# Kernel tuning notes

Hardware: AMD Instinct MI355X
Metric: run time of the kernel (lower is better)

Reference implementation:

```python
import jax, jax.numpy as jnp
import numpy as np

H = 128  # GRU hidden size

def gru_cell(x, h, Wih, Whh, bih, bhh):
    # torch GRU gate order: r, z, n
    gx = x @ Wih.T + bih          # (B, 3H)
    gh = h @ Whh.T + bhh          # (B, 3H)
    xr, xz, xn = jnp.split(gx, 3, axis=-1)
    hr, hz, hn = jnp.split(gh, 3, axis=-1)
    r = jax.nn.sigmoid(xr + hr)
    z = jax.nn.sigmoid(xz + hz)
    n = jnp.tanh(xn + r * hn)
    return (1.0 - z) * n + z * h

def conv2d(x, w, b, stride):
    y = jax.lax.conv_general_dilated(x, w, window_strides=(stride, stride), padding='VALID',
                                     dimension_numbers=('NCHW', 'OIHW', 'NCHW'))
    return y + b[None, :, None, None]

def setup_inputs() -> dict:
    key = jax.random.key(0)
    ks = jax.random.split(key, 20)
    B, T = 8192, 64
    s = lambda *sh: 0.1
    inp = {
        'cnn_states': jax.random.normal(ks[0], (B, 8, 8, 27), jnp.float32),
        'linears_states': jax.random.normal(ks[1], (B, T, 29), jnp.float32),
        'conv1_w': jax.random.normal(ks[2], (16, 27, 3, 3), jnp.float32) * 0.1,
        'conv1_b': jnp.zeros((16,), jnp.float32),
        'conv2_w': jax.random.normal(ks[3], (32, 16, 2, 2), jnp.float32) * 0.1,
        'conv2_b': jnp.zeros((32,), jnp.float32),
        'fc_w': jax.random.normal(ks[4], (128, 128), jnp.float32) * 0.1,
        'fc_b': jnp.zeros((128,), jnp.float32),
        'enc_Wih': jax.random.normal(ks[5], (3 * H, 29), jnp.float32) * 0.1,
        'enc_Whh': jax.random.normal(ks[6], (3 * H, H), jnp.float32) * 0.1,
        'enc_bih': jnp.zeros((3 * H,), jnp.float32),
        'enc_bhh': jnp.zeros((3 * H,), jnp.float32),
        'dec_Wih': jax.random.normal(ks[7], (3 * H, H), jnp.float32) * 0.1,
        'dec_Whh': jax.random.normal(ks[8], (3 * H, H), jnp.float32) * 0.1,
        'dec_bih': jnp.zeros((3 * H,), jnp.float32),
        'dec_bhh': jnp.zeros((3 * H,), jnp.float32),
        'dis_w': jax.random.normal(ks[9], (78, 256), jnp.float32) * 0.01,
        'dis_b': jnp.zeros((78,), jnp.float32),
        'value_w': jax.random.normal(ks[10], (1, 256), jnp.float32) * 0.1,
        'value_b': jnp.zeros((1,), jnp.float32),
    }
    return inp

def _forward(cnn_states, linears_states, conv1_w, conv1_b, conv2_w, conv2_b, fc_w, fc_b,
             enc_Wih, enc_Whh, enc_bih, enc_bhh, dec_Wih, dec_Whh, dec_bih, dec_bhh,
             dis_w, dis_b, value_w, value_b):
    B, T = linears_states.shape[0], linears_states.shape[1]
    # CNN encoder (NHWC -> NCHW)
    x = jnp.transpose(cnn_states, (0, 3, 1, 2))
    x = jax.nn.relu(conv2d(x, conv1_w, conv1_b, 2))   # (B,16,3,3)
    x = jax.nn.relu(conv2d(x, conv2_w, conv2_b, 1))   # (B,32,2,2)
    x = x.reshape(B, -1)                               # (B,128), CHW order matches torch Flatten
    z_cnn = jax.nn.relu(x @ fc_w.T + fc_b)             # (B,128)

    # encoder GRU over linears_states
    xs = jnp.transpose(linears_states, (1, 0, 2))      # (T,B,29)
    h0 = jnp.zeros((B, H), linears_states.dtype)
    def enc_step(h, xt):
        h2 = gru_cell(xt, h, enc_Wih, enc_Whh, enc_bih, enc_bhh)
        return h2, None
    h_enc, _ = jax.lax.scan(enc_step, h0, xs)

    x0 = jnp.zeros((B, H), linears_states.dtype)
    def dec_step(carry, _):
        xin, h = carry
        h2 = gru_cell(xin, h, dec_Wih, dec_Whh, dec_bih, dec_bhh)
        return (h2, h2), None
    (z_pn, _), _ = jax.lax.scan(dec_step, (x0, h_enc), None, length=T)

    pn = jnp.concatenate([z_cnn, z_pn], axis=1)        # (B,256)
    distris = pn @ dis_w.T + dis_b                     # (B,78)
    value = pn @ value_w.T + value_b                   # (B,1)
    return distris, value

def reference(cnn_states, linears_states, conv1_w, conv1_b, conv2_w, conv2_b, fc_w, fc_b,
              enc_Wih, enc_Whh, enc_bih, enc_bhh, dec_Wih, dec_Whh, dec_bih, dec_bhh,
              dis_w, dis_b, value_w, value_b):
    return _forward(cnn_states, linears_states, conv1_w, conv1_b, conv2_w, conv2_b, fc_w, fc_b,
                    enc_Wih, enc_Whh, enc_bih, enc_bhh, dec_Wih, dec_Whh, dec_bih, dec_bhh,
                    dis_w, dis_b, value_w, value_b)
```

## Files before the change

kernel.cpp:

```cpp
#include <hip/hip_runtime.h>

typedef _Float16 f16;
typedef _Float16 f16x8 __attribute__((ext_vector_type(8)));
typedef float f32x4 __attribute__((ext_vector_type(4)));

#define WS_EWIH 4194304
#define WS_EWHH 4218880
#define WS_DWC  4317184
#define WS_DWHH 4448256
#define WS_BIAS 4546560
#define WS_W1F  4550656
#define WS_W2F  4559872
#define WS_FCWF 4563968

static __device__ __forceinline__ f32x4 mfma16(f16x8 a, f16x8 b, f32x4 c) {
    return __builtin_amdgcn_mfma_f32_16x16x32_f16(a, b, c, 0, 0, 0);
}
static __device__ __forceinline__ float fexp2n(float x) {
    return __builtin_amdgcn_exp2f(x * -1.4426950408889634f);
}

__global__ void k_prep(const float* __restrict__ eWih, const float* __restrict__ eWhh,
                       const float* __restrict__ ebih, const float* __restrict__ ebhh,
                       const float* __restrict__ dWih, const float* __restrict__ dWhh,
                       const float* __restrict__ dbih, const float* __restrict__ dbhh,
                       const float* __restrict__ w1, const float* __restrict__ w2,
                       const float* __restrict__ fcw,
                       char* __restrict__ ws)
{
    f16* ewih = (f16*)(ws + WS_EWIH);
    f16* ewhh = (f16*)(ws + WS_EWHH);
    f16* dwc  = (f16*)(ws + WS_DWC);
    f16* dwhh = (f16*)(ws + WS_DWHH);
    float* bias = (float*)(ws + WS_BIAS);
    f16* w1f = (f16*)(ws + WS_W1F);
    f16* w2f = (f16*)(ws + WS_W2F);
    f16* fcwf = (f16*)(ws + WS_FCWF);
    const int total = 12288 + 49152 + 65536 + 49152 + 1024 + 4608 + 2048 + 16384;
    for (int i = blockIdx.x * 256 + threadIdx.x; i < total; i += gridDim.x * 256) {
        int j = i;
        if (j < 12288) { int g = j >> 5, k = j & 31;
            ewih[j] = (f16)((k < 29) ? eWih[g * 29 + k] : 0.0f); continue; }
        j -= 12288;
        if (j < 49152) { ewhh[j] = (f16)eWhh[j]; continue; }
        j -= 49152;
        if (j < 65536) { int row = j >> 7, k = j & 127; float v;
            if (row < 256)      v = dWih[row * 128 + k] + dWhh[row * 128 + k];
            else if (row < 384) v = dWih[row * 128 + k];
            else                v = dWhh[(row - 128) * 128 + k];
            dwc[j] = (f16)v; continue; }
        j -= 65536;
        if (j < 49152) { dwhh[j] = (f16)dWhh[j]; continue; }
        j -= 49152;
        if (j < 1024) {
            if (j < 256)        bias[j] = ebih[j] + ebhh[j];
            else if (j < 384)   bias[j] = ebih[j];
            else if (j < 512)   bias[j] = ebhh[j - 128];
            else if (j < 768)   bias[j] = dbih[j - 512] + dbhh[j - 512];
            else if (j < 896)   bias[j] = dbih[j - 512];
            else                bias[j] = dbhh[j - 640];
            continue; }
        j -= 1024;
        if (j < 4608) {
            int kk = j >> 9, rem = j & 511, co = rem >> 5, k = rem & 31;
            w1f[j] = (f16)((k < 27) ? w1[co * 243 + k * 9 + kk] : 0.0f); continue; }
        j -= 4608;
        if (j < 2048) {
            int s = j >> 10, rem = j & 1023, co = rem >> 5, k = rem & 31;
            int kk2 = 2 * s + (k >= 16), ci = k & 15;
            w2f[j] = (f16)w2[co * 64 + ci * 4 + kk2]; continue; }
        j -= 2048;
        fcwf[j] = (f16)fcw[j];
    }
}

__global__ __launch_bounds__(512, 4) void k_gru(
    const float* __restrict__ cin,
    const float* __restrict__ lin,
    const float* __restrict__ b1, const float* __restrict__ b2,
    const float* __restrict__ fcb,
    const char* __restrict__ ws,
    const float* __restrict__ dis_w, const float* __restrict__ dis_b,
    const float* __restrict__ value_w, const float* __restrict__ value_b,
    float* __restrict__ out)
{
    __shared__ __align__(16) char smem[31488];
    f16 (*a1f)[9][24]  = (f16(*)[9][24])(smem);
    f16 (*x_s)[16][32] = (f16(*)[16][32])(smem + 8192);
    float (*pn_s)[264] = (float(*)[264])(smem + 10240);
    f16 (*vf)[136]     = (f16(*)[136])(smem + 27136);
#define HS(B) (smem + (B) * 4096)

    const int tid = threadIdx.x;
    const int wv = tid >> 6;
    const int lane = tid & 63;
    const int nl = lane & 15;
    const int quad = lane >> 4;
    const int j0 = wv * 16;
    const int row0 = blockIdx.x * 16;

    const f16* ewih = (const f16*)(ws + WS_EWIH);
    const f16* ewhh = (const f16*)(ws + WS_EWHH);
    const f16* dwc  = (const f16*)(ws + WS_DWC);
    const f16* dwhh = (const f16*)(ws + WS_DWHH);
    const float* bias = (const float*)(ws + WS_BIAS);
    const f16* w1f = (const f16*)(ws + WS_W1F);
    const f16* w2f = (const f16*)(ws + WS_W2F);
    const f16* fcwf = (const f16*)(ws + WS_FCWF);

    {
        const float* imgp = cin + (size_t)(row0 + nl) * 1728 + quad * 8;
        float b1v = b1[nl];
        for (int p = wv; p < 9; p += 8) {
            int oy = p / 3, ox = p % 3;
            f32x4 acc = {b1v, b1v, b1v, b1v};
            #pragma unroll
            for (int kk = 0; kk < 9; kk++) {
                f16x8 bw = *(const f16x8*)(w1f + (kk * 16 + nl) * 32 + quad * 8);
                int pix = (2 * oy + kk / 3) * 8 + (2 * ox + kk % 3);
                const float* s = imgp + pix * 27;
                f16x8 a;
                #pragma unroll
                for (int jj = 0; jj < 8; jj++) a[jj] = (f16)s[jj];
                acc = mfma16(a, bw, acc);
            }
            #pragma unroll
            for (int r = 0; r < 4; r++)
                a1f[quad * 4 + r][p][nl] = (f16)fmaxf(acc[r], 0.0f);
        }
        __syncthreads();
        {
            int pos = wv >> 1, nt = wv & 1;
            int y = pos >> 1, x = pos & 1;
            float bv = b2[nt * 16 + nl];
            f32x4 acc = {bv, bv, bv, bv};
            #pragma unroll
            for (int s = 0; s < 2; s++) {
                int kk2 = 2 * s + (quad >> 1);
                int pos1 = (y + (kk2 >> 1)) * 3 + (x + (kk2 & 1));
                f16x8 a = *(const f16x8*)(&a1f[nl][pos1][(quad & 1) * 8]);
                f16x8 b = *(const f16x8*)(w2f + ((size_t)s * 32 + nt * 16 + nl) * 32 + quad * 8);
                acc = mfma16(a, b, acc);
            }
            #pragma unroll
            for (int r = 0; r < 4; r++)
                vf[quad * 4 + r][(nt * 16 + nl) * 4 + (y * 2 + x)] = (f16)fmaxf(acc[r], 0.0f);
        }
        __syncthreads();
        {
            int o = wv * 16 + nl;
            float bv = fcb[o];
            f32x4 acc = {bv, bv, bv, bv};
            #pragma unroll
            for (int kt = 0; kt < 4; kt++) {
                f16x8 a = *(const f16x8*)(&vf[nl][kt * 32 + quad * 8]);
                f16x8 b = *(const f16x8*)(fcwf + o * 128 + kt * 32 + quad * 8);
                acc = mfma16(a, b, acc);
            }
            #pragma unroll
            for (int r = 0; r < 4; r++)
                pn_s[quad * 4 + r][o] = fmaxf(acc[r], 0.0f);
        }
        __syncthreads();
    }

    for (int i = tid; i < 4096; i += 512) ((f16*)smem)[i] = (f16)0.0f;

    const int lane7 = nl & 7;
    int rb[4], wb[4];
    #pragma unroll
    for (int kt = 0; kt < 4; kt++)
        rb[kt] = nl * 256 + (((4 * kt + quad) ^ lane7) << 4);
    #pragma unroll
    for (int r = 0; r < 4; r++) {
        int row = quad * 4 + r;
        wb[r] = row * 256 + ((((2 * wv + (nl >> 3)) ^ (row & 7)) << 3) + lane7) * 2;
    }

    float ho[4];
    #pragma unroll
    for (int r = 0; r < 4; r++) ho[r] = 0.0f;

    const int xr = tid >> 5, xc = tid & 31;
    const bool xok = (xc < 29);
    const size_t lin_base = (size_t)(row0 + xr) * 1856 + xc;

    {
        float eb_r, eb_z, eb_xn, eb_hn;
        { int c = j0 + nl;
          eb_r = bias[c]; eb_z = bias[128 + c]; eb_xn = bias[256 + c]; eb_hn = bias[384 + c]; }
        f16x8 we_r[4], we_z[4], we_hn[4], we_xr, we_xz, we_xn;
        { int gr = j0 + nl;
          #pragma unroll
          for (int kt = 0; kt < 4; kt++) {
              we_r[kt]  = *(const f16x8*)(ewhh + gr * 128 + kt * 32 + quad * 8);
              we_z[kt]  = *(const f16x8*)(ewhh + (128 + gr) * 128 + kt * 32 + quad * 8);
              we_hn[kt] = *(const f16x8*)(ewhh + (256 + gr) * 128 + kt * 32 + quad * 8);
          }
          we_xr = *(const f16x8*)(ewih + gr * 32 + quad * 8);
          we_xz = *(const f16x8*)(ewih + (128 + gr) * 32 + quad * 8);
          we_xn = *(const f16x8*)(ewih + (256 + gr) * 32 + quad * 8);
        }

        float xv = xok ? lin[lin_base] : 0.0f;

#define ENC_STEP(BUF, OBUF, TN)                                                      \
        do {                                                                         \
            x_s[BUF][xr][xc] = (f16)xv;                                              \
            __syncthreads();                                                         \
            f16x8 ax = *(const f16x8*)(&x_s[BUF][nl][quad * 8]);                     \
            f16x8 ah0 = *(const f16x8*)(HS(BUF) + rb[0]);                            \
            f16x8 ah1 = *(const f16x8*)(HS(BUF) + rb[1]);                            \
            f16x8 ah2 = *(const f16x8*)(HS(BUF) + rb[2]);                            \
            f16x8 ah3 = *(const f16x8*)(HS(BUF) + rb[3]);                            \
            if ((TN) < 64) xv = xok ? lin[lin_base + (TN) * 29] : 0.0f;              \
            f32x4 aR  = {eb_r, eb_r, eb_r, eb_r};                                    \
            f32x4 aZ  = {eb_z, eb_z, eb_z, eb_z};                                    \
            f32x4 aXN = {eb_xn, eb_xn, eb_xn, eb_xn};                                \
            f32x4 aHN = {eb_hn, eb_hn, eb_hn, eb_hn};                                \
            aR  = mfma16(ax, we_xr, aR);                                             \
            aZ  = mfma16(ax, we_xz, aZ);                                             \
            aXN = mfma16(ax, we_xn, aXN);                                            \
            aR  = mfma16(ah0, we_r[0], aR);  aR  = mfma16(ah1, we_r[1], aR);         \
            aR  = mfma16(ah2, we_r[2], aR);  aR  = mfma16(ah3, we_r[3], aR);         \
            aZ  = mfma16(ah0, we_z[0], aZ);  aZ  = mfma16(ah1, we_z[1], aZ);         \
            aZ  = mfma16(ah2, we_z[2], aZ);  aZ  = mfma16(ah3, we_z[3], aZ);         \
            aHN = mfma16(ah0, we_hn[0], aHN); aHN = mfma16(ah1, we_hn[1], aHN);      \
            aHN = mfma16(ah2, we_hn[2], aHN); aHN = mfma16(ah3, we_hn[3], aHN);      \
            _Pragma("unroll")                                                        \
            for (int r = 0; r < 4; r++) {                                            \
                float ea = fexp2n(aR[r]), eb = fexp2n(aZ[r]);                        \
                float s1 = 1.0f + ea, s2 = 1.0f + eb;                                \
                float R = __builtin_amdgcn_rcpf(s1 * s2);                            \
                float rg = s2 * R, zg = s1 * R;                                      \
                float ec = fexp2n(2.0f * (aXN[r] + rg * aHN[r]));                    \
                float ng = (1.0f - ec) * __builtin_amdgcn_rcpf(1.0f + ec);           \
                float h = ng + zg * (ho[r] - ng);                                    \
                ho[r] = h;                                                           \
                *(f16*)(HS(OBUF) + wb[r]) = (f16)h;                                  \
            }                                                                        \
        } while (0)

        for (int t = 0; t < 64; t += 2) {
            ENC_STEP(0, 1, t + 1);
            ENC_STEP(1, 0, t + 2);
        }
#undef ENC_STEP
    }

    float db_r, db_z, db_xn, db_hn;
    { int c = j0 + nl;
      db_r = bias[512 + c]; db_z = bias[640 + c]; db_xn = bias[768 + c]; db_hn = bias[896 + c]; }

    {
        __syncthreads();
        f16x8 ah0 = *(const f16x8*)(HS(0) + rb[0]);
        f16x8 ah1 = *(const f16x8*)(HS(0) + rb[1]);
        f16x8 ah2 = *(const f16x8*)(HS(0) + rb[2]);
        f16x8 ah3 = *(const f16x8*)(HS(0) + rb[3]);
        int gr = j0 + nl;
        f32x4 aR  = {db_r, db_r, db_r, db_r};
        f32x4 aZ  = {db_z, db_z, db_z, db_z};
        f32x4 aHN = {db_hn, db_hn, db_hn, db_hn};
        #pragma unroll
        for (int kt = 0; kt < 4; kt++) {
            f16x8 b0 = *(const f16x8*)(dwhh + gr * 128 + kt * 32 + quad * 8);
            f16x8 b1 = *(const f16x8*)(dwhh + (128 + gr) * 128 + kt * 32 + quad * 8);
            f16x8 b2 = *(const f16x8*)(dwhh + (256 + gr) * 128 + kt * 32 + quad * 8);
            f16x8 a = (kt == 0) ? ah0 : (kt == 1) ? ah1 : (kt == 2) ? ah2 : ah3;
            aR  = mfma16(a, b0, aR);
            aZ  = mfma16(a, b1, aZ);
            aHN = mfma16(a, b2, aHN);
        }
        #pragma unroll
        for (int r = 0; r < 4; r++) {
            float ea = fexp2n(aR[r]), eb = fexp2n(aZ[r]);
            float s1 = 1.0f + ea, s2 = 1.0f + eb;
            float R = __builtin_amdgcn_rcpf(s1 * s2);
            float rg = s2 * R, zg = s1 * R;
            float ec = fexp2n(2.0f * (db_xn + rg * aHN[r]));
            float ng = (1.0f - ec) * __builtin_amdgcn_rcpf(1.0f + ec);
            float h = ng + zg * (ho[r] - ng);
            ho[r] = h;
            *(f16*)(HS(1) + wb[r]) = (f16)h;
        }
    }
    {
        f16x8 wd_r[4], wd_z[4], wd_xn[4], wd_hn[4];
        { int gr = j0 + nl;
          #pragma unroll
          for (int kt = 0; kt < 4; kt++) {
              wd_r[kt]  = *(const f16x8*)(dwc + gr * 128 + kt * 32 + quad * 8);
              wd_z[kt]  = *(const f16x8*)(dwc + (128 + gr) * 128 + kt * 32 + quad * 8);
              wd_xn[kt] = *(const f16x8*)(dwc + (256 + gr) * 128 + kt * 32 + quad * 8);
              wd_hn[kt] = *(const f16x8*)(dwc + (384 + gr) * 128 + kt * 32 + quad * 8);
          }
        }

#define DEC_STEP(BUF, OBUF)                                                          \
        do {                                                                         \
            __syncthreads();                                                         \
            f16x8 ah0 = *(const f16x8*)(HS(BUF) + rb[0]);                            \
            f16x8 ah1 = *(const f16x8*)(HS(BUF) + rb[1]);                            \
            f16x8 ah2 = *(const f16x8*)(HS(BUF) + rb[2]);                            \
            f16x8 ah3 = *(const f16x8*)(HS(BUF) + rb[3]);                            \
            f32x4 aR  = {db_r, db_r, db_r, db_r};                                    \
            f32x4 aZ  = {db_z, db_z, db_z, db_z};                                    \
            f32x4 aXN = {db_xn, db_xn, db_xn, db_xn};                                \
            f32x4 aHN = {db_hn, db_hn, db_hn, db_hn};                                \
            aR  = mfma16(ah0, wd_r[0], aR);   aR  = mfma16(ah1, wd_r[1], aR);        \
            aR  = mfma16(ah2, wd_r[2], aR);   aR  = mfma16(ah3, wd_r[3], aR);        \
            aZ  = mfma16(ah0, wd_z[0], aZ);   aZ  = mfma16(ah1, wd_z[1], aZ);        \
            aZ  = mfma16(ah2, wd_z[2], aZ);   aZ  = mfma16(ah3, wd_z[3], aZ);        \
            aXN = mfma16(ah0, wd_xn[0], aXN); aXN = mfma16(ah1, wd_xn[1], aXN);      \
            aXN = mfma16(ah2, wd_xn[2], aXN); aXN = mfma16(ah3, wd_xn[3], aXN);      \
            aHN = mfma16(ah0, wd_hn[0], aHN); aHN = mfma16(ah1, wd_hn[1], aHN);      \
            aHN = mfma16(ah2, wd_hn[2], aHN); aHN = mfma16(ah3, wd_hn[3], aHN);      \
            _Pragma("unroll")                                                        \
            for (int r = 0; r < 4; r++) {                                            \
                float ea = fexp2n(aR[r]), eb = fexp2n(aZ[r]);                        \
                float s1 = 1.0f + ea, s2 = 1.0f + eb;                                \
                float R = __builtin_amdgcn_rcpf(s1 * s2);                            \
                float rg = s2 * R, zg = s1 * R;                                      \
                float ec = fexp2n(2.0f * (aXN[r] + rg * aHN[r]));                    \
                float ng = (1.0f - ec) * __builtin_amdgcn_rcpf(1.0f + ec);           \
                float h = ng + zg * (ho[r] - ng);                                    \
                ho[r] = h;                                                           \
                *(f16*)(HS(OBUF) + wb[r]) = (f16)h;                                  \
            }                                                                        \
        } while (0)

        DEC_STEP(1, 0);
        for (int t = 2; t < 64; t += 2) {
            DEC_STEP(0, 1);
            DEC_STEP(1, 0);
        }
#undef DEC_STEP
    }

    #pragma unroll
    for (int r = 0; r < 4; r++)
        pn_s[quad * 4 + r][128 + j0 + nl] = ho[r];
    __syncthreads();

    const int rr = tid & 15, og = tid >> 4;
    const float4* pr4 = (const float4*)(&pn_s[rr][0]);
    for (int o = og; o < 79; o += 32) {
        const float* wrow_p = (o < 78) ? (dis_w + o * 256) : value_w;
        float acc = (o < 78) ? dis_b[o] : value_b[0];
        const float4* wr4 = (const float4*)wrow_p;
        #pragma unroll 8
        for (int k = 0; k < 64; k++) {
            float4 a = wr4[k], b = pr4[k];
            acc += a.x * b.x + a.y * b.y + a.z * b.z + a.w * b.w;
        }
        if (o < 78) out[(size_t)(row0 + rr) * 78 + o] = acc;
        else        out[(size_t)8192 * 78 + row0 + rr] = acc;
    }
#undef HS
}

extern "C" void kernel_launch(void* const* d_in, const int* in_sizes, int n_in,
                              void* d_out, int out_size, void* d_ws, size_t ws_size,
                              hipStream_t stream)
{
    (void)in_sizes; (void)n_in; (void)out_size; (void)ws_size;
    const float* cnn  = (const float*)d_in[0];
    const float* lin  = (const float*)d_in[1];
    const float* c1w  = (const float*)d_in[2];
    const float* c1b  = (const float*)d_in[3];
    const float* c2w  = (const float*)d_in[4];
    const float* c2b  = (const float*)d_in[5];
    const float* fcw  = (const float*)d_in[6];
    const float* fcb  = (const float*)d_in[7];
    const float* eWih = (const float*)d_in[8];
    const float* eWhh = (const float*)d_in[9];
    const float* ebih = (const float*)d_in[10];
    const float* ebhh = (const float*)d_in[11];
    const float* dWih = (const float*)d_in[12];
    const float* dWhh = (const float*)d_in[13];
    const float* dbih = (const float*)d_in[14];
    const float* dbhh = (const float*)d_in[15];
    const float* disw = (const float*)d_in[16];
    const float* disb = (const float*)d_in[17];
    const float* vw   = (const float*)d_in[18];
    const float* vb   = (const float*)d_in[19];
    char* ws = (char*)d_ws;
    float* out = (float*)d_out;

    hipLaunchKernelGGL(k_prep, dim3(128), dim3(256), 0, stream,
                       eWih, eWhh, ebih, ebhh, dWih, dWhh, dbih, dbhh,
                       c1w, c2w, fcw, ws);
    hipLaunchKernelGGL(k_gru, dim3(512), dim3(512), 0, stream,
                       cnn, lin, c1b, c2b, fcb, ws, disw, disb, vw, vb, out);
}
```

Before: 334.4 us.

## Stage GRU weight fragments through shared memory with coalesced loads

```diff
diff --git a/kernel.cpp b/kernel.cpp
--- a/kernel.cpp
+++ b/kernel.cpp
@@ -74,7 +74,7 @@
     }
 }
 
-__global__ __launch_bounds__(512, 4) void k_gru(
+__global__ __launch_bounds__(512, 2) void k_gru(
     const float* __restrict__ cin,
     const float* __restrict__ lin,
     const float* __restrict__ b1, const float* __restrict__ b2,
@@ -84,11 +84,12 @@
     const float* __restrict__ value_w, const float* __restrict__ value_b,
     float* __restrict__ out)
 {
-    __shared__ __align__(16) char smem[31488];
+    __shared__ __align__(16) char smem[47360];
     f16 (*a1f)[9][24]  = (f16(*)[9][24])(smem);
     f16 (*x_s)[16][32] = (f16(*)[16][32])(smem + 8192);
+    char* wstage       = smem + 10240;
     float (*pn_s)[264] = (float(*)[264])(smem + 10240);
-    f16 (*vf)[136]     = (f16(*)[136])(smem + 27136);
+    f16 (*vf)[136]     = (f16(*)[136])(smem + 43008);
 #define HS(B) (smem + (B) * 4096)
 
     const int tid = threadIdx.x;
@@ -107,6 +108,8 @@
     const f16* w1f = (const f16*)(ws + WS_W1F);
     const f16* w2f = (const f16*)(ws + WS_W2F);
     const f16* fcwf = (const f16*)(ws + WS_FCWF);
+
+    float zc[4];
 
     {
         const float* imgp = cin + (size_t)(row0 + nl) * 1728 + quad * 8;
@@ -159,7 +162,7 @@
             }
             #pragma unroll
             for (int r = 0; r < 4; r++)
-                pn_s[quad * 4 + r][o] = fmaxf(acc[r], 0.0f);
+                zc[r] = fmaxf(acc[r], 0.0f);
         }
         __syncthreads();
     }
@@ -177,6 +180,8 @@
         wb[r] = row * 256 + ((((2 * wv + (nl >> 3)) ^ (row & 7)) << 3) + lane7) * 2;
     }
 
+    const int frag_off0 = ((j0 + nl) * 128) * 2 + (quad * 8) * 2;
+
     float ho[4];
     #pragma unroll
     for (int r = 0; r < 4; r++) ho[r] = 0.0f;
@@ -189,17 +194,32 @@
         float eb_r, eb_z, eb_xn, eb_hn;
         { int c = j0 + nl;
           eb_r = bias[c]; eb_z = bias[128 + c]; eb_xn = bias[256 + c]; eb_hn = bias[384 + c]; }
+
         f16x8 we_r[4], we_z[4], we_hn[4], we_xr, we_xz, we_xn;
-        { int gr = j0 + nl;
-          #pragma unroll
-          for (int kt = 0; kt < 4; kt++) {
-              we_r[kt]  = *(const f16x8*)(ewhh + gr * 128 + kt * 32 + quad * 8);
-              we_z[kt]  = *(const f16x8*)(ewhh + (128 + gr) * 128 + kt * 32 + quad * 8);
-              we_hn[kt] = *(const f16x8*)(ewhh + (256 + gr) * 128 + kt * 32 + quad * 8);
-          }
-          we_xr = *(const f16x8*)(ewih + gr * 32 + quad * 8);
-          we_xz = *(const f16x8*)(ewih + (128 + gr) * 32 + quad * 8);
-          we_xn = *(const f16x8*)(ewih + (256 + gr) * 32 + quad * 8);
+        {
+            __syncthreads();
+            for (int i = tid * 16; i < 24576; i += 512 * 16)
+                *(f16x8*)(wstage + i) = *(const f16x8*)((const char*)ewih + i);
+            __syncthreads();
+            we_xr = *(const f16x8*)(wstage + ((j0 + nl) * 32 + quad * 8) * 2);
+            we_xz = *(const f16x8*)(wstage + ((128 + j0 + nl) * 32 + quad * 8) * 2);
+            we_xn = *(const f16x8*)(wstage + ((256 + j0 + nl) * 32 + quad * 8) * 2);
+            #pragma unroll
+            for (int g = 0; g < 3; g++) {
+                __syncthreads();
+                const char* src = (const char*)(ewhh + g * 128 * 128);
+                for (int i = tid * 16; i < 32768; i += 512 * 16)
+                    *(f16x8*)(wstage + i) = *(const f16x8*)(src + i);
+                __syncthreads();
+                #pragma unroll
+                for (int kt = 0; kt < 4; kt++) {
+                    f16x8 v = *(const f16x8*)(wstage + frag_off0 + kt * 64);
+                    if (g == 0) we_r[kt] = v;
+                    else if (g == 1) we_z[kt] = v;
+                    else we_hn[kt] = v;
+                }
+            }
+            __syncthreads();
         }
 
         float xv = xok ? lin[lin_base] : 0.0f;
@@ -287,14 +307,21 @@
     }
     {
         f16x8 wd_r[4], wd_z[4], wd_xn[4], wd_hn[4];
-        { int gr = j0 + nl;
-          #pragma unroll
-          for (int kt = 0; kt < 4; kt++) {
-              wd_r[kt]  = *(const f16x8*)(dwc + gr * 128 + kt * 32 + quad * 8);
-              wd_z[kt]  = *(const f16x8*)(dwc + (128 + gr) * 128 + kt * 32 + quad * 8);
-              wd_xn[kt] = *(const f16x8*)(dwc + (256 + gr) * 128 + kt * 32 + quad * 8);
-              wd_hn[kt] = *(const f16x8*)(dwc + (384 + gr) * 128 + kt * 32 + quad * 8);
-          }
+        #pragma unroll
+        for (int g = 0; g < 4; g++) {
+            __syncthreads();
+            const char* src = (const char*)(dwc + g * 128 * 128);
+            for (int i = tid * 16; i < 32768; i += 512 * 16)
+                *(f16x8*)(wstage + i) = *(const f16x8*)(src + i);
+            __syncthreads();
+            #pragma unroll
+            for (int kt = 0; kt < 4; kt++) {
+                f16x8 v = *(const f16x8*)(wstage + frag_off0 + kt * 64);
+                if (g == 0) wd_r[kt] = v;
+                else if (g == 1) wd_z[kt] = v;
+                else if (g == 2) wd_xn[kt] = v;
+                else wd_hn[kt] = v;
+            }
         }
 
 #define DEC_STEP(BUF, OBUF)                                                          \
@@ -338,9 +365,12 @@
 #undef DEC_STEP
     }
 
+    __syncthreads();
     #pragma unroll
-    for (int r = 0; r < 4; r++)
+    for (int r = 0; r < 4; r++) {
+        pn_s[quad * 4 + r][wv * 16 + nl] = zc[r];
         pn_s[quad * 4 + r][128 + j0 + nl] = ho[r];
+    }
     __syncthreads();
 
     const int rr = tid & 15, og = tid >> 4;
```

Measured after the change: 369.3 us. +10.4%, slower.

## Process two independent 16-row batch tiles per block to interleave GRU recurrences

Applied to the files above, without the earlier changes.

```diff
diff --git a/kernel.cpp b/kernel.cpp
--- a/kernel.cpp
+++ b/kernel.cpp
@@ -74,7 +74,7 @@
     }
 }
 
-__global__ __launch_bounds__(512, 4) void k_gru(
+__global__ __launch_bounds__(512, 2) void k_gru(
     const float* __restrict__ cin,
     const float* __restrict__ lin,
     const float* __restrict__ b1, const float* __restrict__ b2,
@@ -84,12 +84,14 @@
     const float* __restrict__ value_w, const float* __restrict__ value_b,
     float* __restrict__ out)
 {
-    __shared__ __align__(16) char smem[31488];
+    __shared__ __align__(16) char smem[62976];
     f16 (*a1f)[9][24]  = (f16(*)[9][24])(smem);
-    f16 (*x_s)[16][32] = (f16(*)[16][32])(smem + 8192);
-    float (*pn_s)[264] = (float(*)[264])(smem + 10240);
-    f16 (*vf)[136]     = (f16(*)[136])(smem + 27136);
-#define HS(B) (smem + (B) * 4096)
+    float (*pn_s)[264] = (float(*)[264])(smem + 20480);
+    f16 (*vf)[136]     = (f16(*)[136])(smem + 54272);
+#define HSA(B) (smem + (B) * 4096)
+#define HSB(B) (smem + 8192 + (B) * 4096)
+#define XSA(B) ((f16(*)[32])(smem + 16384 + (B) * 1024))
+#define XSB(B) ((f16(*)[32])(smem + 18432 + (B) * 1024))
 
     const int tid = threadIdx.x;
     const int wv = tid >> 6;
@@ -97,7 +99,7 @@
     const int nl = lane & 15;
     const int quad = lane >> 4;
     const int j0 = wv * 16;
-    const int row0 = blockIdx.x * 16;
+    const int row0 = blockIdx.x * 32;
 
     const f16* ewih = (const f16*)(ws + WS_EWIH);
     const f16* ewhh = (const f16*)(ws + WS_EWHH);
@@ -108,11 +110,14 @@
     const f16* w2f = (const f16*)(ws + WS_W2F);
     const f16* fcwf = (const f16*)(ws + WS_FCWF);
 
+    float zc[2][4];
+
     {
-        const float* imgp = cin + (size_t)(row0 + nl) * 1728 + quad * 8;
         float b1v = b1[nl];
-        for (int p = wv; p < 9; p += 8) {
+        for (int p2 = wv; p2 < 18; p2 += 8) {
+            int g = p2 / 9, p = p2 % 9;
             int oy = p / 3, ox = p % 3;
+            const float* imgp = cin + (size_t)(row0 + g * 16 + nl) * 1728 + quad * 8;
             f32x4 acc = {b1v, b1v, b1v, b1v};
             #pragma unroll
             for (int kk = 0; kk < 9; kk++) {
@@ -126,11 +131,11 @@
             }
             #pragma unroll
             for (int r = 0; r < 4; r++)
-                a1f[quad * 4 + r][p][nl] = (f16)fmaxf(acc[r], 0.0f);
+                a1f[g * 16 + quad * 4 + r][p][nl] = (f16)fmaxf(acc[r], 0.0f);
         }
         __syncthreads();
-        {
-            int pos = wv >> 1, nt = wv & 1;
+        for (int u = wv; u < 16; u += 8) {
+            int g = u >> 3, pos = (u & 7) >> 1, nt = u & 1;
             int y = pos >> 1, x = pos & 1;
             float bv = b2[nt * 16 + nl];
             f32x4 acc = {bv, bv, bv, bv};
@@ -138,33 +143,34 @@
             for (int s = 0; s < 2; s++) {
                 int kk2 = 2 * s + (quad >> 1);
                 int pos1 = (y + (kk2 >> 1)) * 3 + (x + (kk2 & 1));
-                f16x8 a = *(const f16x8*)(&a1f[nl][pos1][(quad & 1) * 8]);
+                f16x8 a = *(const f16x8*)(&a1f[g * 16 + nl][pos1][(quad & 1) * 8]);
                 f16x8 b = *(const f16x8*)(w2f + ((size_t)s * 32 + nt * 16 + nl) * 32 + quad * 8);
                 acc = mfma16(a, b, acc);
             }
             #pragma unroll
             for (int r = 0; r < 4; r++)
-                vf[quad * 4 + r][(nt * 16 + nl) * 4 + (y * 2 + x)] = (f16)fmaxf(acc[r], 0.0f);
+                vf[g * 16 + quad * 4 + r][(nt * 16 + nl) * 4 + (y * 2 + x)] = (f16)fmaxf(acc[r], 0.0f);
         }
         __syncthreads();
-        {
+        #pragma unroll
+        for (int g = 0; g < 2; g++) {
             int o = wv * 16 + nl;
             float bv = fcb[o];
             f32x4 acc = {bv, bv, bv, bv};
             #pragma unroll
             for (int kt = 0; kt < 4; kt++) {
-                f16x8 a = *(const f16x8*)(&vf[nl][kt * 32 + quad * 8]);
+                f16x8 a = *(const f16x8*)(&vf[g * 16 + nl][kt * 32 + quad * 8]);
                 f16x8 b = *(const f16x8*)(fcwf + o * 128 + kt * 32 + quad * 8);
                 acc = mfma16(a, b, acc);
             }
             #pragma unroll
             for (int r = 0; r < 4; r++)
-                pn_s[quad * 4 + r][o] = fmaxf(acc[r], 0.0f);
+                zc[g][r] = fmaxf(acc[r], 0.0f);
         }
         __syncthreads();
     }
 
-    for (int i = tid; i < 4096; i += 512) ((f16*)smem)[i] = (f16)0.0f;
+    for (int i = tid; i < 8192; i += 512) ((f16*)smem)[i] = (f16)0.0f;
 
     const int lane7 = nl & 7;
     int rb[4], wb[4];
@@ -177,13 +183,28 @@
         wb[r] = row * 256 + ((((2 * wv + (nl >> 3)) ^ (row & 7)) << 3) + lane7) * 2;
     }
 
-    float ho[4];
+    float hoA[4], hoB[4];
     #pragma unroll
-    for (int r = 0; r < 4; r++) ho[r] = 0.0f;
+    for (int r = 0; r < 4; r++) { hoA[r] = 0.0f; hoB[r] = 0.0f; }
 
     const int xr = tid >> 5, xc = tid & 31;
     const bool xok = (xc < 29);
-    const size_t lin_base = (size_t)(row0 + xr) * 1856 + xc;
+    const size_t lin_baseA = (size_t)(row0 + xr) * 1856 + xc;
+    const size_t lin_baseB = (size_t)(row0 + 16 + xr) * 1856 + xc;
+
+#define EW4(aR, aZ, aXN, aHN, ho, HDST)                                              \
+        _Pragma("unroll")                                                            \
+        for (int r = 0; r < 4; r++) {                                                \
+            float ea = fexp2n(aR[r]), eb = fexp2n(aZ[r]);                            \
+            float s1 = 1.0f + ea, s2 = 1.0f + eb;                                    \
+            float R = __builtin_amdgcn_rcpf(s1 * s2);                                \
+            float rg = s2 * R, zg = s1 * R;                                          \
+            float ec = fexp2n(2.0f * (aXN[r] + rg * aHN[r]));                        \
+            float ng = (1.0f - ec) * __builtin_amdgcn_rcpf(1.0f + ec);               \
+            float h = ng + zg * (ho[r] - ng);                                        \
+            ho[r] = h;                                                               \
+            *(f16*)((HDST) + wb[r]) = (f16)h;                                        \
+        }
 
     {
         float eb_r, eb_z, eb_xn, eb_hn;
@@ -202,43 +223,49 @@
           we_xn = *(const f16x8*)(ewih + (256 + gr) * 32 + quad * 8);
         }
 
-        float xv = xok ? lin[lin_base] : 0.0f;
+        float xvA = xok ? lin[lin_baseA] : 0.0f;
+        float xvB = xok ? lin[lin_baseB] : 0.0f;
 
 #define ENC_STEP(BUF, OBUF, TN)                                                      \
         do {                                                                         \
-            x_s[BUF][xr][xc] = (f16)xv;                                              \
+            XSA(BUF)[xr][xc] = (f16)xvA;                                             \
+            XSB(BUF)[xr][xc] = (f16)xvB;                                             \
             __syncthreads();                                                         \
-            f16x8 ax = *(const f16x8*)(&x_s[BUF][nl][quad * 8]);                     \
-            f16x8 ah0 = *(const f16x8*)(HS(BUF) + rb[0]);                            \
-            f16x8 ah1 = *(const f16x8*)(HS(BUF) + rb[1]);                            \
-            f16x8 ah2 = *(const f16x8*)(HS(BUF) + rb[2]);                            \
-            f16x8 ah3 = *(const f16x8*)(HS(BUF) + rb[3]);                            \
-            if ((TN) < 64) xv = xok ? lin[lin_base + (TN) * 29] : 0.0f;              \
-            f32x4 aR  = {eb_r, eb_r, eb_r, eb_r};                                    \
-            f32x4 aZ  = {eb_z, eb_z, eb_z, eb_z};                                    \
-            f32x4 aXN = {eb_xn, eb_xn, eb_xn, eb_xn};                                \
-            f32x4 aHN = {eb_hn, eb_hn, eb_hn, eb_hn};                                \
-            aR  = mfma16(ax, we_xr, aR);                                             \
-            aZ  = mfma16(ax, we_xz, aZ);                                             \
-            aXN = mfma16(ax, we_xn, aXN);                                            \
-            aR  = mfma16(ah0, we_r[0], aR);  aR  = mfma16(ah1, we_r[1], aR);         \
-            aR  = mfma16(ah2, we_r[2], aR);  aR  = mfma16(ah3, we_r[3], aR);         \
-            aZ  = mfma16(ah0, we_z[0], aZ);  aZ  = mfma16(ah1, we_z[1], aZ);         \
-            aZ  = mfma16(ah2, we_z[2], aZ);  aZ  = mfma16(ah3, we_z[3], aZ);         \
-            aHN = mfma16(ah0, we_hn[0], aHN); aHN = mfma16(ah1, we_hn[1], aHN);      \
-            aHN = mfma16(ah2, we_hn[2], aHN); aHN = mfma16(ah3, we_hn[3], aHN);      \
-            _Pragma("unroll")                                                        \
-            for (int r = 0; r < 4; r++) {                                            \
-                float ea = fexp2n(aR[r]), eb = fexp2n(aZ[r]);                        \
-                float s1 = 1.0f + ea, s2 = 1.0f + eb;                                \
-                float R = __builtin_amdgcn_rcpf(s1 * s2);                            \
-                float rg = s2 * R, zg = s1 * R;                                      \
-                float ec = fexp2n(2.0f * (aXN[r] + rg * aHN[r]));                    \
-                float ng = (1.0f - ec) * __builtin_amdgcn_rcpf(1.0f + ec);           \
-                float h = ng + zg * (ho[r] - ng);                                    \
-                ho[r] = h;                                                           \
-                *(f16*)(HS(OBUF) + wb[r]) = (f16)h;                                  \
+            f16x8 axA = *(const f16x8*)(&XSA(BUF)[nl][quad * 8]);                    \
+            f16x8 axB = *(const f16x8*)(&XSB(BUF)[nl][quad * 8]);                    \
+            f16x8 aA0 = *(const f16x8*)(HSA(BUF) + rb[0]);                           \
+            f16x8 aA1 = *(const f16x8*)(HSA(BUF) + rb[1]);                           \
+            f16x8 aA2 = *(const f16x8*)(HSA(BUF) + rb[2]);                           \
+            f16x8 aA3 = *(const f16x8*)(HSA(BUF) + rb[3]);                           \
+            f16x8 aB0 = *(const f16x8*)(HSB(BUF) + rb[0]);                           \
+            f16x8 aB1 = *(const f16x8*)(HSB(BUF) + rb[1]);                           \
+            f16x8 aB2 = *(const f16x8*)(HSB(BUF) + rb[2]);                           \
+            f16x8 aB3 = *(const f16x8*)(HSB(BUF) + rb[3]);                           \
+            if ((TN) < 64) {                                                         \
+                xvA = xok ? lin[lin_baseA + (TN) * 29] : 0.0f;                       \
+                xvB = xok ? lin[lin_baseB + (TN) * 29] : 0.0f;                       \
             }                                                                        \
+            f32x4 RA = {eb_r, eb_r, eb_r, eb_r},  RB = RA;                           \
+            f32x4 ZA = {eb_z, eb_z, eb_z, eb_z},  ZB = ZA;                           \
+            f32x4 XNA = {eb_xn, eb_xn, eb_xn, eb_xn}, XNB = XNA;                     \
+            f32x4 HNA = {eb_hn, eb_hn, eb_hn, eb_hn}, HNB = HNA;                     \
+            RA  = mfma16(axA, we_xr, RA);   RB  = mfma16(axB, we_xr, RB);            \
+            ZA  = mfma16(axA, we_xz, ZA);   ZB  = mfma16(axB, we_xz, ZB);            \
+            XNA = mfma16(axA, we_xn, XNA);  XNB = mfma16(axB, we_xn, XNB);           \
+            RA  = mfma16(aA0, we_r[0], RA);   RB  = mfma16(aB0, we_r[0], RB);        \
+            RA  = mfma16(aA1, we_r[1], RA);   RB  = mfma16(aB1, we_r[1], RB);        \
+            RA  = mfma16(aA2, we_r[2], RA);   RB  = mfma16(aB2, we_r[2], RB);        \
+            RA  = mfma16(aA3, we_r[3], RA);   RB  = mfma16(aB3, we_r[3], RB);        \
+            ZA  = mfma16(aA0, we_z[0], ZA);   ZB  = mfma16(aB0, we_z[0], ZB);        \
+            ZA  = mfma16(aA1, we_z[1], ZA);   ZB  = mfma16(aB1, we_z[1], ZB);        \
+            ZA  = mfma16(aA2, we_z[2], ZA);   ZB  = mfma16(aB2, we_z[2], ZB);        \
+            ZA  = mfma16(aA3, we_z[3], ZA);   ZB  = mfma16(aB3, we_z[3], ZB);        \
+            HNA = mfma16(aA0, we_hn[0], HNA); HNB = mfma16(aB0, we_hn[0], HNB);      \
+            HNA = mfma16(aA1, we_hn[1], HNA); HNB = mfma16(aB1, we_hn[1], HNB);      \
+            HNA = mfma16(aA2, we_hn[2], HNA); HNB = mfma16(aB2, we_hn[2], HNB);      \
+            HNA = mfma16(aA3, we_hn[3], HNA); HNB = mfma16(aB3, we_hn[3], HNB);      \
+            EW4(RA, ZA, XNA, HNA, hoA, HSA(OBUF))                                    \
+            EW4(RB, ZB, XNB, HNB, hoB, HSB(OBUF))                                    \
         } while (0)
 
         for (int t = 0; t < 64; t += 2) {
@@ -254,36 +281,32 @@
 
     {
         __syncthreads();
-        f16x8 ah0 = *(const f16x8*)(HS(0) + rb[0]);
-        f16x8 ah1 = *(const f16x8*)(HS(0) + rb[1]);
-        f16x8 ah2 = *(const f16x8*)(HS(0) + rb[2]);
-        f16x8 ah3 = *(const f16x8*)(HS(0) + rb[3]);
+        f16x8 aA0 = *(const f16x8*)(HSA(0) + rb[0]);
+        f16x8 aA1 = *(const f16x8*)(HSA(0) + rb[1]);
+        f16x8 aA2 = *(const f16x8*)(HSA(0) + rb[2]);
+        f16x8 aA3 = *(const f16x8*)(HSA(0) + rb[3]);
+        f16x8 aB0 = *(const f16x8*)(HSB(0) + rb[0]);
+        f16x8 aB1 = *(const f16x8*)(HSB(0) + rb[1]);
+        f16x8 aB2 = *(const f16x8*)(HSB(0) + rb[2]);
+        f16x8 aB3 = *(const f16x8*)(HSB(0) + rb[3]);
         int gr = j0 + nl;
-        f32x4 aR  = {db_r, db_r, db_r, db_r};
-        f32x4 aZ  = {db_z, db_z, db_z, db_z};
-        f32x4 aHN = {db_hn, db_hn, db_hn, db_hn};
+        f32x4 RA = {db_r, db_r, db_r, db_r},  RB = RA;
+        f32x4 ZA = {db_z, db_z, db_z, db_z},  ZB = ZA;
+        f32x4 XNA = {db_xn, db_xn, db_xn, db_xn}, XNB = XNA;
+        f32x4 HNA = {db_hn, db_hn, db_hn, db_hn}, HNB = HNA;
         #pragma unroll
         for (int kt = 0; kt < 4; kt++) {
             f16x8 b0 = *(const f16x8*)(dwhh + gr * 128 + kt * 32 + quad * 8);
             f16x8 b1 = *(const f16x8*)(dwhh + (128 + gr) * 128 + kt * 32 + quad * 8);
             f16x8 b2 = *(const f16x8*)(dwhh + (256 + gr) * 128 + kt * 32 + quad * 8);
-            f16x8 a = (kt == 0) ? ah0 : (kt == 1) ? ah1 : (kt == 2) ? ah2 : ah3;
-            aR  = mfma16(a, b0, aR);
-            aZ  = mfma16(a, b1, aZ);
-            aHN = mfma16(a, b2, aHN);
-        }
-        #pragma unroll
-        for (int r = 0; r < 4; r++) {
-            float ea = fexp2n(aR[r]), eb = fexp2n(aZ[r]);
-            float s1 = 1.0f + ea, s2 = 1.0f + eb;
-            float R = __builtin_amdgcn_rcpf(s1 * s2);
-            float rg = s2 * R, zg = s1 * R;
-            float ec = fexp2n(2.0f * (db_xn + rg * aHN[r]));
-            float ng = (1.0f - ec) * __builtin_amdgcn_rcpf(1.0f + ec);
-            float h = ng + zg * (ho[r] - ng);
-            ho[r] = h;
-            *(f16*)(HS(1) + wb[r]) = (f16)h;
-        }
+            f16x8 aA = (kt == 0) ? aA0 : (kt == 1) ? aA1 : (kt == 2) ? aA2 : aA3;
+            f16x8 aB = (kt == 0) ? aB0 : (kt == 1) ? aB1 : (kt == 2) ? aB2 : aB3;
+            RA  = mfma16(aA, b0, RA);   RB  = mfma16(aB, b0, RB);
+            ZA  = mfma16(aA, b1, ZA);   ZB  = mfma16(aB, b1, ZB);
+            HNA = mfma16(aA, b2, HNA);  HNB = mfma16(aB, b2, HNB);
+        }
+        EW4(RA, ZA, XNA, HNA, hoA, HSA(1))
+        EW4(RB, ZB, XNB, HNB, hoB, HSB(1))
     }
     {
         f16x8 wd_r[4], wd_z[4], wd_xn[4], wd_hn[4];
@@ -300,34 +323,36 @@
 #define DEC_STEP(BUF, OBUF)                                                          \
         do {                                                                         \
             __syncthreads();                                                         \
-            f16x8 ah0 = *(const f16x8*)(HS(BUF) + rb[0]);                            \
-            f16x8 ah1 = *(const f16x8*)(HS(BUF) + rb[1]);                            \
-            f16x8 ah2 = *(const f16x8*)(HS(BUF) + rb[2]);                            \
-            f16x8 ah3 = *(const f16x8*)(HS(BUF) + rb[3]);                            \
-            f32x4 aR  = {db_r, db_r, db_r, db_r};                                    \
-            f32x4 aZ  = {db_z, db_z, db_z, db_z};                                    \
-            f32x4 aXN = {db_xn, db_xn, db_xn, db_xn};                                \
-            f32x4 aHN = {db_hn, db_hn, db_hn, db_hn};                                \
-            aR  = mfma16(ah0, wd_r[0], aR);   aR  = mfma16(ah1, wd_r[1], aR);        \
-            aR  = mfma16(ah2, wd_r[2], aR);   aR  = mfma16(ah3, wd_r[3], aR);        \
-            aZ  = mfma16(ah0, wd_z[0], aZ);   aZ  = mfma16(ah1, wd_z[1], aZ);        \
-            aZ  = mfma16(ah2, wd_z[2], aZ);   aZ  = mfma16(ah3, wd_z[3], aZ);        \
-            aXN = mfma16(ah0, wd_xn[0], aXN); aXN = mfma16(ah1, wd_xn[1], aXN);      \
-            aXN = mfma16(ah2, wd_xn[2], aXN); aXN = mfma16(ah3, wd_xn[3], aXN);      \
-            aHN = mfma16(ah0, wd_hn[0], aHN); aHN = mfma16(ah1, wd_hn[1], aHN);      \
-            aHN = mfma16(ah2, wd_hn[2], aHN); aHN = mfma16(ah3, wd_hn[3], aHN);      \
-            _Pragma("unroll")                                                        \
-            for (int r = 0; r < 4; r++) {                                            \
-                float ea = fexp2n(aR[r]), eb = fexp2n(aZ[r]);                        \
-                float s1 = 1.0f + ea, s2 = 1.0f + eb;                                \
-                float R = __builtin_amdgcn_rcpf(s1 * s2);                            \
-                float rg = s2 * R, zg = s1 * R;                                      \
-                float ec = fexp2n(2.0f * (aXN[r] + rg * aHN[r]));                    \
-                float ng = (1.0f - ec) * __builtin_amdgcn_rcpf(1.0f + ec);           \
-                float h = ng + zg * (ho[r] - ng);                                    \
-                ho[r] = h;                                                           \
-                *(f16*)(HS(OBUF) + wb[r]) = (f16)h;                                  \
-            }                                                                        \
+            f16x8 aA0 = *(const f16x8*)(HSA(BUF) + rb[0]);                           \
+            f16x8 aA1 = *(const f16x8*)(HSA(BUF) + rb[1]);                           \
+            f16x8 aA2 = *(const f16x8*)(HSA(BUF) + rb[2]);                           \
+            f16x8 aA3 = *(const f16x8*)(HSA(BUF) + rb[3]);                           \
+            f16x8 aB0 = *(const f16x8*)(HSB(BUF) + rb[0]);                           \
+            f16x8 aB1 = *(const f16x8*)(HSB(BUF) + rb[1]);                           \
+            f16x8 aB2 = *(const f16x8*)(HSB(BUF) + rb[2]);                           \
+            f16x8 aB3 = *(const f16x8*)(HSB(BUF) + rb[3]);                           \
+            f32x4 RA = {db_r, db_r, db_r, db_r},  RB = RA;                           \
+            f32x4 ZA = {db_z, db_z, db_z, db_z},  ZB = ZA;                           \
+            f32x4 XNA = {db_xn, db_xn, db_xn, db_xn}, XNB = XNA;                     \
+            f32x4 HNA = {db_hn, db_hn, db_hn, db_hn}, HNB = HNA;                     \
+            RA  = mfma16(aA0, wd_r[0], RA);   RB  = mfma16(aB0, wd_r[0], RB);        \
+            RA  = mfma16(aA1, wd_r[1], RA);   RB  = mfma16(aB1, wd_r[1], RB);        \
+            RA  = mfma16(aA2, wd_r[2], RA);   RB  = mfma16(aB2, wd_r[2], RB);        \
+            RA  = mfma16(aA3, wd_r[3], RA);   RB  = mfma16(aB3, wd_r[3], RB);        \
+            ZA  = mfma16(aA0, wd_z[0], ZA);   ZB  = mfma16(aB0, wd_z[0], ZB);        \
+            ZA  = mfma16(aA1, wd_z[1], ZA);   ZB  = mfma16(aB1, wd_z[1], ZB);        \
+            ZA  = mfma16(aA2, wd_z[2], ZA);   ZB  = mfma16(aB2, wd_z[2], ZB);        \
+            ZA  = mfma16(aA3, wd_z[3], ZA);   ZB  = mfma16(aB3, wd_z[3], ZB);        \
+            XNA = mfma16(aA0, wd_xn[0], XNA); XNB = mfma16(aB0, wd_xn[0], XNB);      \
+            XNA = mfma16(aA1, wd_xn[1], XNA); XNB = mfma16(aB1, wd_xn[1], XNB);      \
+            XNA = mfma16(aA2, wd_xn[2], XNA); XNB = mfma16(aB2, wd_xn[2], XNB);      \
+            XNA = mfma16(aA3, wd_xn[3], XNA); XNB = mfma16(aB3, wd_xn[3], XNB);      \
+            HNA = mfma16(aA0, wd_hn[0], HNA); HNB = mfma16(aB0, wd_hn[0], HNB);      \
+            HNA = mfma16(aA1, wd_hn[1], HNA); HNB = mfma16(aB1, wd_hn[1], HNB);      \
+            HNA = mfma16(aA2, wd_hn[2], HNA); HNB = mfma16(aB2, wd_hn[2], HNB);      \
+            HNA = mfma16(aA3, wd_hn[3], HNA); HNB = mfma16(aB3, wd_hn[3], HNB);      \
+            EW4(RA, ZA, XNA, HNA, hoA, HSA(OBUF))                                    \
+            EW4(RB, ZB, XNB, HNB, hoB, HSB(OBUF))                                    \
         } while (0)
 
         DEC_STEP(1, 0);
@@ -338,14 +363,19 @@
 #undef DEC_STEP
     }
 
+    __syncthreads();
     #pragma unroll
-    for (int r = 0; r < 4; r++)
-        pn_s[quad * 4 + r][128 + j0 + nl] = ho[r];
+    for (int r = 0; r < 4; r++) {
+        pn_s[quad * 4 + r][wv * 16 + nl] = zc[0][r];
+        pn_s[16 + quad * 4 + r][wv * 16 + nl] = zc[1][r];
+        pn_s[quad * 4 + r][128 + j0 + nl] = hoA[r];
+        pn_s[16 + quad * 4 + r][128 + j0 + nl] = hoB[r];
+    }
     __syncthreads();
 
-    const int rr = tid & 15, og = tid >> 4;
+    const int rr = tid & 31, og = tid >> 5;
     const float4* pr4 = (const float4*)(&pn_s[rr][0]);
-    for (int o = og; o < 79; o += 32) {
+    for (int o = og; o < 79; o += 16) {
         const float* wrow_p = (o < 78) ? (dis_w + o * 256) : value_w;
         float acc = (o < 78) ? dis_b[o] : value_b[0];
         const float4* wr4 = (const float4*)wrow_p;
@@ -357,7 +387,11 @@
         if (o < 78) out[(size_t)(row0 + rr) * 78 + o] = acc;
         else        out[(size_t)8192 * 78 + row0 + rr] = acc;
     }
-#undef HS
+#undef HSA
+#undef HSB
+#undef XSA
+#undef XSB
+#undef EW4
 }
 
 extern "C" void kernel_launch(void* const* d_in, const int* in_sizes, int n_in,
@@ -391,6 +425,6 @@
     hipLaunchKernelGGL(k_prep, dim3(128), dim3(256), 0, stream,
                        eWih, eWhh, ebih, ebhh, dWih, dWhh, dbih, dbhh,
                        c1w, c2w, fcw, ws);
-    hipLaunchKernelGGL(k_gru, dim3(512), dim3(512), 0, stream,
+    hipLaunchKernelGGL(k_gru, dim3(256), dim3(512), 0, stream,
                        cnn, lin, c1b, c2b, fcb, ws, disw, disb, vw, vb, out);
 }
```

Measured after the change: 340.6 us. Within noise of the previous version (+1.8%).
